# Kernel optimization log

Hardware: AMD Instinct MI355X
Metric: run time of the kernel (lower is better)

## Reference

```python
import jax, jax.numpy as jnp
import numpy as np

B, T, D, H = 4, 2048, 1024, 16
DK = D // H
LN_EPS = 1e-5


def setup_inputs() -> dict:
    key = jax.random.key(0)
    ks = jax.random.split(key, 12)
    s = 1.0 / np.sqrt(D)
    inp = {
        'x': jax.random.normal(ks[0], (B, T, D), jnp.float32),
        'Wq': jax.random.normal(ks[1], (D, D), jnp.float32) * s,
        'bq': jnp.zeros((D,), jnp.float32),
        'Wk': jax.random.normal(ks[2], (D, D), jnp.float32) * s,
        'bk': jnp.zeros((D,), jnp.float32),
        'Wv': jax.random.normal(ks[3], (D, D), jnp.float32) * s,
        'bv': jnp.zeros((D,), jnp.float32),
        'Wo': jax.random.normal(ks[4], (D, D), jnp.float32) * s,
        'bo': jnp.zeros((D,), jnp.float32),
        'ln_g': jnp.ones((D,), jnp.float32),
        'ln_b': jnp.zeros((D,), jnp.float32),
    }
    return inp


def reference(x, Wq, bq, Wk, bk, Wv, bv, Wo, bo, ln_g, ln_b):
    b, t, d = x.shape
    scale = jnp.sqrt(jnp.asarray(DK, x.dtype))
    # QKV projections -> [b, h, t, dk]
    q = (x @ Wq + bq).reshape(b, t, H, DK).transpose(0, 2, 1, 3)
    k = (x @ Wk + bk).reshape(b, t, H, DK).transpose(0, 2, 1, 3)
    v = (x @ Wv + bv).reshape(b, t, H, DK).transpose(0, 2, 1, 3)
    scores = jnp.einsum('bhqd,bhkd->bhqk', q, k) / scale  # [b,h,t,t]
    mask = jnp.tril(jnp.ones((t, t), x.dtype))[None, None]  # [1,1,t,t]
    neg = jnp.finfo(x.dtype).min
    scores = jnp.where(mask == 0, neg, scores)
    attn = jax.nn.softmax(scores, axis=-1)
    # mask-renormalize (as in the torch module)
    attn = attn * mask
    denom = attn.sum(-1, keepdims=True)
    attn = jnp.where(denom > 0, attn / denom, jnp.zeros_like(attn))
    ctx = jnp.einsum('bhqk,bhkd->bhqd', attn, v)  # [b,h,t,dk]
    ctx = ctx.transpose(0, 2, 1, 3).reshape(b, t, d)
    out = ctx @ Wo + bo
    y = out + x  # residual
    mu = y.mean(-1, keepdims=True)
    var = ((y - mu) ** 2).mean(-1, keepdims=True)
    return (y - mu) / jnp.sqrt(var + LN_EPS) * ln_g + ln_b
```

## Files before the change

### kernel.cpp

```cpp
#include <hip/hip_runtime.h>


using u16 = unsigned short;
using u32 = unsigned int;
typedef _Float16 f16x8 __attribute__((ext_vector_type(8)));
typedef __fp16 h16x2 __attribute__((ext_vector_type(2)));
typedef float f32x4 __attribute__((ext_vector_type(4)));
typedef unsigned short u16x8 __attribute__((ext_vector_type(8)));
typedef unsigned short u16x4 __attribute__((ext_vector_type(4)));
typedef unsigned int u32x4 __attribute__((ext_vector_type(4)));

template <bool B> struct BoolTag { static constexpr bool v = B; };

__device__ inline u16 f2h_bits(float f) {
    _Float16 h = (_Float16)f;
    return __builtin_bit_cast(u16, h);
}
__device__ inline float h2f(u16 u) {
    return (float)__builtin_bit_cast(_Float16, u);
}

__device__ __forceinline__ void gload16(const void* g, void* l) {
    __builtin_amdgcn_global_load_lds(
        (const __attribute__((address_space(1))) void*)g,
        (__attribute__((address_space(3))) void*)l, 16, 0, 0);
}

__global__ __launch_bounds__(256) void convert_kernel(
    const float* __restrict__ x, u16* __restrict__ xb,
    const float* __restrict__ W0, const float* __restrict__ W1,
    const float* __restrict__ W2, const float* __restrict__ W3,
    u16* __restrict__ Wt) {
    __shared__ float ts[64][68];
    const int bid = blockIdx.x, tid = threadIdx.x;
    if (bid < 4096) {
        size_t i = ((size_t)bid * 256 + tid) * 8;
        float4 a = *(const float4*)(x + i);
        float4 b = *(const float4*)(x + i + 4);
        u16x8 o;
        o[0] = f2h_bits(a.x); o[1] = f2h_bits(a.y); o[2] = f2h_bits(a.z); o[3] = f2h_bits(a.w);
        o[4] = f2h_bits(b.x); o[5] = f2h_bits(b.y); o[6] = f2h_bits(b.z); o[7] = f2h_bits(b.w);
        *(u16x8*)(xb + i) = o;
        return;
    }
    const int wb = bid - 4096;
    const int z = wb >> 8, rem = wb & 255;
    const float* W = z == 0 ? W0 : (z == 1 ? W1 : (z == 2 ? W2 : W3));
    u16* Wo = Wt + (size_t)z * 1048576;
    const int k0 = (rem >> 4) * 64, n0 = (rem & 15) * 64;
    const int rr = tid >> 3, c = tid & 7;
#pragma unroll
    for (int p = 0; p < 2; p++) {
        int k = p * 32 + rr;
        float4 u = *(const float4*)(W + (size_t)(k0 + k) * 1024 + n0 + c * 8);
        float4 w = *(const float4*)(W + (size_t)(k0 + k) * 1024 + n0 + c * 8 + 4);
        *(float4*)&ts[k][c * 8] = u;
        *(float4*)&ts[k][c * 8 + 4] = w;
    }
    __syncthreads();
#pragma unroll
    for (int p = 0; p < 2; p++) {
        int n = p * 32 + rr;
        u16 o[8];
#pragma unroll
        for (int j = 0; j < 8; j++) o[j] = f2h_bits(ts[c * 8 + j][n]);
        *(u16x8*)(Wo + (size_t)(n0 + n) * 1024 + k0 + c * 8) = *(u16x8*)o;
    }
}

template <int MODE>
__global__ __launch_bounds__(256) void gemm128_kernel(
    const u16* __restrict__ A, const u16* __restrict__ Wt,
    const float* __restrict__ b0, const float* __restrict__ b1,
    const float* __restrict__ b2, u16* __restrict__ qo, u16* __restrict__ ko,
    u16* __restrict__ vt) {
    constexpr int NBY = (MODE == 0) ? 24 : 8;
    __shared__ u16 SH[32768];

    const int bid = blockIdx.x;
    const int cpx = (MODE == 0) ? 192 : 64;
    const int swz = (bid & 7) * cpx + (bid >> 3);
    const int bx = swz / NBY, by = swz % NBY;
    const size_t row0 = (size_t)bx * 128;
    const size_t col0 = (size_t)by * 128;

    const int tid = threadIdx.x, lane = tid & 63;
    const int wid = tid >> 6, wm = wid >> 1, wn = wid & 1;
    const int l15 = lane & 15, lg = lane >> 4;
    const int rr = tid >> 3, c8 = tid & 7;
    const int scw = (c8 ^ (rr & 7)) * 8;

    f32x4 acc[4][4] = {};

    auto stage_tile = [&](int kt, int p) {
        const int k0 = kt * 64;
        u16* dA = SH + p * 8192;
        u16* dB = SH + 16384 + p * 8192;
#pragma unroll
        for (int g = 0; g < 4; g++) {
            gload16(A + (row0 + g * 32 + rr) * 1024 + k0 + scw,
                    dA + (g * 256 + tid) * 8);
            gload16(Wt + (col0 + g * 32 + rr) * 1024 + k0 + scw,
                    dB + (g * 256 + tid) * 8);
        }
    };

    auto ldops = [&](int p, int kcv, f16x8* Af, f16x8* Bf) {
        const u16* bA = SH + p * 8192;
        const u16* bB = SH + 16384 + p * 8192;
        const int swo = ((kcv * 4 + lg) ^ (l15 & 7)) * 8;
#pragma unroll
        for (int n = 0; n < 4; n++)
            Bf[n] = *(const f16x8*)(bB + (wn * 64 + n * 16 + l15) * 64 + swo);
#pragma unroll
        for (int m = 0; m < 4; m++)
            Af[m] = *(const f16x8*)(bA + (wm * 64 + m * 16 + l15) * 64 + swo);
    };

    auto domfma = [&](const f16x8* Af, const f16x8* Bf) {
        __builtin_amdgcn_s_setprio(1);
#pragma unroll
        for (int m = 0; m < 4; m++)
#pragma unroll
            for (int n = 0; n < 4; n++)
                acc[m][n] = __builtin_amdgcn_mfma_f32_16x16x32_f16(
                    Af[m], Bf[n], acc[m][n], 0, 0, 0);
        __builtin_amdgcn_s_setprio(0);
    };

    stage_tile(0, 0);
    asm volatile("s_waitcnt vmcnt(0)" ::: "memory");
    __builtin_amdgcn_sched_barrier(0);
    __builtin_amdgcn_s_barrier();

#pragma unroll 1
    for (int t = 0; t < 16; t++) {
        const int cp = t & 1, np = (t + 1) & 1;
        f16x8 af[4], bf[4];
        ldops(cp, 0, af, bf);
        if (t < 15) stage_tile(t + 1, np);
        __builtin_amdgcn_sched_barrier(0);
        __builtin_amdgcn_s_barrier();
        asm volatile("s_waitcnt lgkmcnt(0)" ::: "memory");
        __builtin_amdgcn_sched_barrier(0);
        domfma(af, bf);
        __builtin_amdgcn_sched_barrier(0);
        __builtin_amdgcn_s_barrier();
        ldops(cp, 1, af, bf);
        if (t < 15) asm volatile("s_waitcnt vmcnt(0)" ::: "memory");
        __builtin_amdgcn_sched_barrier(0);
        __builtin_amdgcn_s_barrier();
        asm volatile("s_waitcnt lgkmcnt(0)" ::: "memory");
        __builtin_amdgcn_sched_barrier(0);
        domfma(af, bf);
        __builtin_amdgcn_sched_barrier(0);
        if (t < 15) __builtin_amdgcn_s_barrier();
    }

    if (MODE == 0) {
        const int zsel = by >> 3;
        if (zsel < 2) {
            u16* ob = zsel == 0 ? qo : ko;
            const float* bias = zsel == 0 ? b0 : b1;
            const float qs = zsel == 0 ? 0.18033688f : 1.0f;
#pragma unroll
            for (int m = 0; m < 4; m++) {
#pragma unroll
                for (int n = 0; n < 4; n++) {
                    size_t col = col0 + wn * 64 + n * 16 + l15;
                    size_t colz = col & 1023;
                    float bb = bias[colz];
#pragma unroll
                    for (int r = 0; r < 4; r++) {
                        size_t row = row0 + wm * 64 + m * 16 + lg * 4 + r;
                        ob[row * 1024 + colz] = f2h_bits((acc[m][n][r] + bb) * qs);
                    }
                }
            }
        } else {
            u16* TL = SH;
            const int dz0 = (by - 16) * 128;
            __syncthreads();
#pragma unroll
            for (int m = 0; m < 4; m++) {
#pragma unroll
                for (int n = 0; n < 4; n++) {
                    int cl = wn * 64 + n * 16 + l15;
                    float bb = b2[dz0 + cl];
#pragma unroll
                    for (int r = 0; r < 4; r++) {
                        int rl = wm * 64 + m * 16 + lg * 4 + r;
                        TL[cl * 134 + rl] = f2h_bits(acc[m][n][r] + bb);
                    }
                }
            }
            __syncthreads();
            const int vcl = tid >> 1, th = tid & 1;
            const int b = (int)(row0 >> 11);
            const int tloc = (int)(row0 & 2047);
            size_t vrow = (size_t)b * 1024 + dz0 + vcl;
#pragma unroll
            for (int j = 0; j < 8; j++)
                *(u16x8*)(vt + vrow * 2048 + tloc + th * 64 + j * 8) =
                    *(const u16x8*)(TL + vcl * 134 + th * 64 + j * 8);
        }
    } else {
        u16* yo = qo;
        const u16* xres = ko;
#pragma unroll
        for (int m = 0; m < 4; m++) {
#pragma unroll
            for (int n = 0; n < 4; n++) {
                size_t col = col0 + wn * 64 + n * 16 + l15;
                float bb = b0[col];
#pragma unroll
                for (int r = 0; r < 4; r++) {
                    size_t row = row0 + wm * 64 + m * 16 + lg * 4 + r;
                    size_t idx = row * 1024 + col;
                    yo[idx] = f2h_bits(acc[m][n][r] + bb + h2f(xres[idx]));
                }
            }
        }
    }
}

__global__ __launch_bounds__(512) void attn_kernel(const u16* __restrict__ Q,
                                                   const u16* __restrict__ Kb,
                                                   const u16* __restrict__ Vt,
                                                   u16* __restrict__ ctx) {
    __shared__ u16 Ks[2][128 * 64];
    __shared__ u16 Vs[2][64 * 128];

    const int i = (int)blockIdx.x;
    const int bh = i & 63;
    const int sel = (i >> 6) & 3;
    const int qb = (i < 256) ? (7 - sel) : sel;
    const int b = bh >> 4, h = bh & 15;
    const int tid = threadIdx.x, lane = tid & 63, wid = tid >> 6;
    const int l15 = lane & 15, lg = lane >> 4;
    const int q0w = qb * 256 + wid * 32;
    const int send = qb * 256;

    const int rr = tid >> 3, c8 = tid & 7;
    const int scw = (c8 ^ (rr & 7)) * 8;
    const int vr = tid >> 4, vc = tid & 15;
    const int scv = (vc ^ (vr & 15)) * 8;
    const size_t kbase = ((size_t)b * 2048) * 1024 + h * 64 + scw;
    const size_t vbase0 = ((size_t)bh * 64 + vr) * 2048 + scv;
    const size_t vbase1 = ((size_t)bh * 64 + vr + 32) * 2048 + scv;

    f16x8 qv[2][2];
#pragma unroll
    for (int qf = 0; qf < 2; qf++) {
        size_t qoff = ((size_t)b * 2048 + q0w + qf * 16 + l15) * 1024 + h * 64 + lg * 8;
        qv[qf][0] = *(const f16x8*)(Q + qoff);
        qv[qf][1] = *(const f16x8*)(Q + qoff + 32);
    }

    const int swk0 = (lg ^ (l15 & 7)) * 8;
    const int swk1 = ((4 + lg) ^ (l15 & 7)) * 8;

    const h16x2 one2 = {(__fp16)1.0f, (__fp16)1.0f};

    f32x4 acc[2][4] = {};
    float psum[2] = {0.0f, 0.0f};

    auto stage = [&](int s, int bf) {
        gload16(Kb + kbase + (size_t)(s + rr) * 1024, Ks[bf] + tid * 8);
        gload16(Kb + kbase + (size_t)(s + rr + 64) * 1024, Ks[bf] + (512 + tid) * 8);
        gload16(Vt + vbase0 + s, Vs[bf] + tid * 8);
        gload16(Vt + vbase1 + s, Vs[bf] + (512 + tid) * 8);
    };

    auto body = [&](int s, int bf, auto maskc) {
        constexpr bool MASK = decltype(maskc)::v;
        u32 W[2][8][2];
#pragma unroll
        for (int c = 0; c < 8; c++) {
            const u16* kp = Ks[bf] + (c * 16 + l15) * 64;
            f16x8 kf0 = *(const f16x8*)(kp + swk0);
            f16x8 kf1 = *(const f16x8*)(kp + swk1);
#pragma unroll
            for (int qf = 0; qf < 2; qf++) {
                f32x4 z = {};
                z = __builtin_amdgcn_mfma_f32_16x16x32_f16(kf0, qv[qf][0], z, 0, 0, 0);
                z = __builtin_amdgcn_mfma_f32_16x16x32_f16(kf1, qv[qf][1], z, 0, 0, 0);
                float p0 = __builtin_amdgcn_exp2f(z[0]);
                float p1 = __builtin_amdgcn_exp2f(z[1]);
                float p2 = __builtin_amdgcn_exp2f(z[2]);
                float p3 = __builtin_amdgcn_exp2f(z[3]);
                if (MASK) {
                    int kk = s + c * 16 + lg * 4;
                    int qq = q0w + qf * 16 + l15;
                    p0 = (kk + 0 <= qq) ? p0 : 0.0f;
                    p1 = (kk + 1 <= qq) ? p1 : 0.0f;
                    p2 = (kk + 2 <= qq) ? p2 : 0.0f;
                    p3 = (kk + 3 <= qq) ? p3 : 0.0f;
                }
                h16x2 w0 = __builtin_amdgcn_cvt_pkrtz(p0, p1);
                h16x2 w1 = __builtin_amdgcn_cvt_pkrtz(p2, p3);
                psum[qf] = __builtin_amdgcn_fdot2(w0, one2, psum[qf], false);
                psum[qf] = __builtin_amdgcn_fdot2(w1, one2, psum[qf], false);
                W[qf][c][0] = __builtin_bit_cast(u32, w0);
                W[qf][c][1] = __builtin_bit_cast(u32, w1);
            }
        }
        f16x8 pa0[2][2], pa1[2][2];
#pragma unroll
        for (int qf = 0; qf < 2; qf++) {
#pragma unroll
            for (int hf = 0; hf < 2; hf++) {
                const int c0 = hf * 4;
                auto sA = __builtin_amdgcn_permlane32_swap(W[qf][c0][0], W[qf][c0 + 1][0], false, false);
                auto tA = __builtin_amdgcn_permlane16_swap(sA[0], sA[1], false, false);
                auto sB = __builtin_amdgcn_permlane32_swap(W[qf][c0][1], W[qf][c0 + 1][1], false, false);
                auto tB = __builtin_amdgcn_permlane16_swap(sB[0], sB[1], false, false);
                u32x4 v0 = {tA[0], tB[0], tA[1], tB[1]};
                pa0[qf][hf] = __builtin_bit_cast(f16x8, v0);
                auto sC = __builtin_amdgcn_permlane32_swap(W[qf][c0 + 2][0], W[qf][c0 + 3][0], false, false);
                auto tC = __builtin_amdgcn_permlane16_swap(sC[0], sC[1], false, false);
                auto sD = __builtin_amdgcn_permlane32_swap(W[qf][c0 + 2][1], W[qf][c0 + 3][1], false, false);
                auto tD = __builtin_amdgcn_permlane16_swap(sD[0], sD[1], false, false);
                u32x4 v1 = {tC[0], tD[0], tC[1], tD[1]};
                pa1[qf][hf] = __builtin_bit_cast(f16x8, v1);
            }
        }
        __builtin_amdgcn_s_setprio(1);
#pragma unroll
        for (int dt = 0; dt < 4; dt++) {
            const u16* vp = Vs[bf] + (dt * 16 + l15) * 128;
#pragma unroll
            for (int hf = 0; hf < 2; hf++) {
                f16x8 vf0 = *(const f16x8*)(vp + ((hf * 8 + lg) ^ l15) * 8);
                f16x8 vf1 = *(const f16x8*)(vp + ((hf * 8 + 4 + lg) ^ l15) * 8);
#pragma unroll
                for (int qf = 0; qf < 2; qf++) {
                    acc[qf][dt] = __builtin_amdgcn_mfma_f32_16x16x32_f16(
                        pa0[qf][hf], vf0, acc[qf][dt], 0, 0, 0);
                    acc[qf][dt] = __builtin_amdgcn_mfma_f32_16x16x32_f16(
                        pa1[qf][hf], vf1, acc[qf][dt], 0, 0, 0);
                }
            }
        }
        __builtin_amdgcn_s_setprio(0);
    };

    stage(0, 0);
    stage(128, 1);
    asm volatile("s_waitcnt vmcnt(4)" ::: "memory");
    __builtin_amdgcn_sched_barrier(0);
    __builtin_amdgcn_s_barrier();

    int cur = 0;
#pragma unroll 1
    for (int s = 0; s < send; s += 128) {
        body(s, cur, BoolTag<false>{});
        __builtin_amdgcn_sched_barrier(0);
        __builtin_amdgcn_s_barrier();
        stage(s + 256, cur);
        asm volatile("s_waitcnt vmcnt(4)" ::: "memory");
        __builtin_amdgcn_sched_barrier(0);
        __builtin_amdgcn_s_barrier();
        cur ^= 1;
    }
    body(send, cur, BoolTag<true>{});
    __builtin_amdgcn_sched_barrier(0);
    __builtin_amdgcn_s_barrier();
    asm volatile("s_waitcnt vmcnt(0)" ::: "memory");
    __builtin_amdgcn_sched_barrier(0);
    __builtin_amdgcn_s_barrier();
    if (wid >= 4) body(send + 128, cur ^ 1, BoolTag<true>{});

#pragma unroll
    for (int qf = 0; qf < 2; qf++) {
        psum[qf] += __shfl_xor(psum[qf], 16);
        psum[qf] += __shfl_xor(psum[qf], 32);
    }
#pragma unroll
    for (int qf = 0; qf < 2; qf++) {
        float inv = 1.0f / psum[qf];
#pragma unroll
        for (int r = 0; r < 4; r++) {
            float ir = __shfl(inv, lg * 4 + r);
            size_t row = (size_t)b * 2048 + q0w + qf * 16 + lg * 4 + r;
#pragma unroll
            for (int dt = 0; dt < 4; dt++)
                ctx[row * 1024 + h * 64 + dt * 16 + l15] = f2h_bits(acc[qf][dt][r] * ir);
        }
    }
}

__global__ __launch_bounds__(256) void ln_kernel(const u16* __restrict__ y,
                                                 const float* __restrict__ g,
                                                 const float* __restrict__ bb,
                                                 float* __restrict__ out) {
    const int r = blockIdx.x, tid = threadIdx.x;
    u16x4 v4 = *(const u16x4*)(y + (size_t)r * 1024 + tid * 4);
    float vx = h2f(v4[0]), vy = h2f(v4[1]), vz = h2f(v4[2]), vw = h2f(v4[3]);
    float s = vx + vy + vz + vw;
    float sq = vx * vx + vy * vy + vz * vz + vw * vw;
#pragma unroll
    for (int ofs = 1; ofs < 64; ofs <<= 1) {
        s += __shfl_xor(s, ofs);
        sq += __shfl_xor(sq, ofs);
    }
    __shared__ float as[4], aq[4];
    if ((tid & 63) == 0) { as[tid >> 6] = s; aq[tid >> 6] = sq; }
    __syncthreads();
    s = as[0] + as[1] + as[2] + as[3];
    sq = aq[0] + aq[1] + aq[2] + aq[3];
    float mu = s * (1.0f / 1024.0f);
    float var = sq * (1.0f / 1024.0f) - mu * mu;
    float rstd = rsqrtf(var + 1e-5f);
    float4 gv = *(const float4*)(g + tid * 4);
    float4 bv = *(const float4*)(bb + tid * 4);
    float4 o4;
    o4.x = (vx - mu) * rstd * gv.x + bv.x;
    o4.y = (vy - mu) * rstd * gv.y + bv.y;
    o4.z = (vz - mu) * rstd * gv.z + bv.z;
    o4.w = (vw - mu) * rstd * gv.w + bv.w;
    *(float4*)(out + (size_t)r * 1024 + tid * 4) = o4;
}

extern "C" void kernel_launch(void* const* d_in, const int* in_sizes, int n_in,
                              void* d_out, int out_size, void* d_ws, size_t ws_size,
                              hipStream_t stream) {
    const float* x  = (const float*)d_in[0];
    const float* Wq = (const float*)d_in[1];
    const float* bq = (const float*)d_in[2];
    const float* Wk = (const float*)d_in[3];
    const float* bk = (const float*)d_in[4];
    const float* Wv = (const float*)d_in[5];
    const float* bv = (const float*)d_in[6];
    const float* Wo = (const float*)d_in[7];
    const float* bo = (const float*)d_in[8];
    const float* lg = (const float*)d_in[9];
    const float* lb = (const float*)d_in[10];
    float* out = (float*)d_out;

    char* ws = (char*)d_ws;
    u16* xb = (u16*)(ws + 0);
    u16* wt = (u16*)(ws + 16777216);
    u16* q  = (u16*)(ws + 25165824);
    u16* k  = (u16*)(ws + 41943040);
    u16* vt = (u16*)(ws + 75497472);
    u16* cx = (u16*)(ws + 92274688);
    u16* y16 = (u16*)(ws + 109051904);

    convert_kernel<<<5120, 256, 0, stream>>>(x, xb, Wq, Wk, Wv, Wo, wt);

    gemm128_kernel<0><<<1536, 256, 0, stream>>>(xb, wt, bq, bk, bv, q, k, vt);
    attn_kernel<<<512, 512, 0, stream>>>(q, k, vt, cx);
    gemm128_kernel<1><<<512, 256, 0, stream>>>(cx, wt + 3145728, bo, nullptr,
                                               nullptr, y16, xb, nullptr);
    ln_kernel<<<8192, 256, 0, stream>>>(y16, lg, lb, out);
}
```

Before: 169.0 us.

## Give output-projection GEMM a dedicated 128x256 tile kernel with triple-buffered loads

Splits the templated GEMM into a QKV kernel and a new output-projection kernel. The new kernel uses 512 threads, 128x256 tiles (256 blocks) and a three-stage LDS ring that prefetches two k-tiles ahead in halves. The aim is more reuse of the A tile and deeper latency hiding for the Wo GEMM. In exchange it launches only 256 blocks, about one wave on the GPU, and uses much more LDS per block.

```diff
diff --git a/kernel.cpp b/kernel.cpp
--- a/kernel.cpp
+++ b/kernel.cpp
@@ -68,19 +68,16 @@
     }
 }
 
-template <int MODE>
-__global__ __launch_bounds__(256) void gemm128_kernel(
+__global__ __launch_bounds__(256) void gemm_qkv128_kernel(
     const u16* __restrict__ A, const u16* __restrict__ Wt,
     const float* __restrict__ b0, const float* __restrict__ b1,
     const float* __restrict__ b2, u16* __restrict__ qo, u16* __restrict__ ko,
     u16* __restrict__ vt) {
-    constexpr int NBY = (MODE == 0) ? 24 : 8;
     __shared__ u16 SH[32768];
 
     const int bid = blockIdx.x;
-    const int cpx = (MODE == 0) ? 192 : 64;
-    const int swz = (bid & 7) * cpx + (bid >> 3);
-    const int bx = swz / NBY, by = swz % NBY;
+    const int swz = (bid & 7) * 192 + (bid >> 3);
+    const int bx = swz / 24, by = swz % 24;
     const size_t row0 = (size_t)bx * 128;
     const size_t col0 = (size_t)by * 128;
 
@@ -157,68 +154,161 @@
         if (t < 15) __builtin_amdgcn_s_barrier();
     }
 
-    if (MODE == 0) {
-        const int zsel = by >> 3;
-        if (zsel < 2) {
-            u16* ob = zsel == 0 ? qo : ko;
-            const float* bias = zsel == 0 ? b0 : b1;
-            const float qs = zsel == 0 ? 0.18033688f : 1.0f;
-#pragma unroll
-            for (int m = 0; m < 4; m++) {
-#pragma unroll
-                for (int n = 0; n < 4; n++) {
-                    size_t col = col0 + wn * 64 + n * 16 + l15;
-                    size_t colz = col & 1023;
-                    float bb = bias[colz];
-#pragma unroll
-                    for (int r = 0; r < 4; r++) {
-                        size_t row = row0 + wm * 64 + m * 16 + lg * 4 + r;
-                        ob[row * 1024 + colz] = f2h_bits((acc[m][n][r] + bb) * qs);
-                    }
+    const int zsel = by >> 3;
+    if (zsel < 2) {
+        u16* ob = zsel == 0 ? qo : ko;
+        const float* bias = zsel == 0 ? b0 : b1;
+        const float qs = zsel == 0 ? 0.18033688f : 1.0f;
+#pragma unroll
+        for (int m = 0; m < 4; m++) {
+#pragma unroll
+            for (int n = 0; n < 4; n++) {
+                size_t col = col0 + wn * 64 + n * 16 + l15;
+                size_t colz = col & 1023;
+                float bb = bias[colz];
+#pragma unroll
+                for (int r = 0; r < 4; r++) {
+                    size_t row = row0 + wm * 64 + m * 16 + lg * 4 + r;
+                    ob[row * 1024 + colz] = f2h_bits((acc[m][n][r] + bb) * qs);
                 }
             }
-        } else {
-            u16* TL = SH;
-            const int dz0 = (by - 16) * 128;
-            __syncthreads();
-#pragma unroll
-            for (int m = 0; m < 4; m++) {
-#pragma unroll
-                for (int n = 0; n < 4; n++) {
-                    int cl = wn * 64 + n * 16 + l15;
-                    float bb = b2[dz0 + cl];
-#pragma unroll
-                    for (int r = 0; r < 4; r++) {
-                        int rl = wm * 64 + m * 16 + lg * 4 + r;
-                        TL[cl * 134 + rl] = f2h_bits(acc[m][n][r] + bb);
-                    }
+        }
+    } else {
+        u16* TL = SH;
+        const int dz0 = (by - 16) * 128;
+        __syncthreads();
+#pragma unroll
+        for (int m = 0; m < 4; m++) {
+#pragma unroll
+            for (int n = 0; n < 4; n++) {
+                int cl = wn * 64 + n * 16 + l15;
+                float bb = b2[dz0 + cl];
+#pragma unroll
+                for (int r = 0; r < 4; r++) {
+                    int rl = wm * 64 + m * 16 + lg * 4 + r;
+                    TL[cl * 134 + rl] = f2h_bits(acc[m][n][r] + bb);
                 }
             }
-            __syncthreads();
-            const int vcl = tid >> 1, th = tid & 1;
-            const int b = (int)(row0 >> 11);
-            const int tloc = (int)(row0 & 2047);
-            size_t vrow = (size_t)b * 1024 + dz0 + vcl;
-#pragma unroll
-            for (int j = 0; j < 8; j++)
-                *(u16x8*)(vt + vrow * 2048 + tloc + th * 64 + j * 8) =
-                    *(const u16x8*)(TL + vcl * 134 + th * 64 + j * 8);
-        }
-    } else {
-        u16* yo = qo;
-        const u16* xres = ko;
-#pragma unroll
-        for (int m = 0; m < 4; m++) {
-#pragma unroll
-            for (int n = 0; n < 4; n++) {
-                size_t col = col0 + wn * 64 + n * 16 + l15;
-                float bb = b0[col];
-#pragma unroll
-                for (int r = 0; r < 4; r++) {
-                    size_t row = row0 + wm * 64 + m * 16 + lg * 4 + r;
-                    size_t idx = row * 1024 + col;
-                    yo[idx] = f2h_bits(acc[m][n][r] + bb + h2f(xres[idx]));
-                }
+        }
+        __syncthreads();
+        const int vcl = tid >> 1, th = tid & 1;
+        const int b = (int)(row0 >> 11);
+        const int tloc = (int)(row0 & 2047);
+        size_t vrow = (size_t)b * 1024 + dz0 + vcl;
+#pragma unroll
+        for (int j = 0; j < 8; j++)
+            *(u16x8*)(vt + vrow * 2048 + tloc + th * 64 + j * 8) =
+                *(const u16x8*)(TL + vcl * 134 + th * 64 + j * 8);
+    }
+}
+
+__global__ __launch_bounds__(512) void gemm_wo_kernel(
+    const u16* __restrict__ A, const u16* __restrict__ Wt,
+    const float* __restrict__ b0, u16* __restrict__ yo,
+    const u16* __restrict__ xres) {
+    __shared__ u16 As[3][128 * 64];
+    __shared__ u16 Bs[3][256 * 64];
+
+    const int bid = blockIdx.x;
+    const int swz = (bid & 7) * 32 + (bid >> 3);
+    const int bx = swz / 4, by = swz % 4;
+    const size_t row0 = (size_t)bx * 128;
+    const size_t col0 = (size_t)by * 256;
+
+    const int tid = threadIdx.x, lane = tid & 63;
+    const int wid = tid >> 6, wm = wid >> 2, wn = wid & 3;
+    const int l15 = lane & 15, lg = lane >> 4;
+    const int rr = tid >> 3, c8 = tid & 7;
+    const int scw = (c8 ^ (rr & 7)) * 8;
+
+    f32x4 acc[4][4] = {};
+
+    auto stage_half = [&](int kt, u16* dA, u16* dB, int h) {
+        const int k0 = kt * 64;
+        if (h == 0) {
+            gload16(A + (row0 + rr) * 1024 + k0 + scw, dA + tid * 8);
+            gload16(Wt + (col0 + rr) * 1024 + k0 + scw, dB + tid * 8);
+            gload16(Wt + (col0 + 64 + rr) * 1024 + k0 + scw, dB + (512 + tid) * 8);
+        } else {
+            gload16(A + (row0 + 64 + rr) * 1024 + k0 + scw, dA + (512 + tid) * 8);
+            gload16(Wt + (col0 + 128 + rr) * 1024 + k0 + scw, dB + (1024 + tid) * 8);
+            gload16(Wt + (col0 + 192 + rr) * 1024 + k0 + scw, dB + (1536 + tid) * 8);
+        }
+    };
+
+    auto ldops = [&](const u16* bA, const u16* bB, int kcv, f16x8* Af, f16x8* Bf) {
+        const int swo = ((kcv * 4 + lg) ^ (l15 & 7)) * 8;
+#pragma unroll
+        for (int n = 0; n < 4; n++)
+            Bf[n] = *(const f16x8*)(bB + (wn * 64 + n * 16 + l15) * 64 + swo);
+#pragma unroll
+        for (int m = 0; m < 4; m++)
+            Af[m] = *(const f16x8*)(bA + (wm * 64 + m * 16 + l15) * 64 + swo);
+    };
+
+    auto domfma = [&](const f16x8* Af, const f16x8* Bf) {
+        __builtin_amdgcn_s_setprio(1);
+#pragma unroll
+        for (int m = 0; m < 4; m++)
+#pragma unroll
+            for (int n = 0; n < 4; n++)
+                acc[m][n] = __builtin_amdgcn_mfma_f32_16x16x32_f16(
+                    Af[m], Bf[n], acc[m][n], 0, 0, 0);
+        __builtin_amdgcn_s_setprio(0);
+    };
+
+    u16 *pA = &As[0][0], *pnA = &As[1][0], *ppA = &As[2][0];
+    u16 *pB = &Bs[0][0], *pnB = &Bs[1][0], *ppB = &Bs[2][0];
+
+    stage_half(0, pA, pB, 0);
+    stage_half(0, pA, pB, 1);
+    stage_half(1, pnA, pnB, 0);
+    stage_half(1, pnA, pnB, 1);
+    asm volatile("s_waitcnt vmcnt(6)" ::: "memory");
+    __builtin_amdgcn_sched_barrier(0);
+    __builtin_amdgcn_s_barrier();
+
+#pragma unroll 1
+    for (int t = 0; t < 16; t++) {
+        f16x8 af[4], bf[4];
+        ldops(pA, pB, 0, af, bf);
+        if (t < 14) stage_half(t + 2, ppA, ppB, 0);
+        __builtin_amdgcn_sched_barrier(0);
+        __builtin_amdgcn_s_barrier();
+        asm volatile("s_waitcnt lgkmcnt(0)" ::: "memory");
+        __builtin_amdgcn_sched_barrier(0);
+        domfma(af, bf);
+        __builtin_amdgcn_sched_barrier(0);
+        __builtin_amdgcn_s_barrier();
+        ldops(pA, pB, 1, af, bf);
+        if (t < 14) stage_half(t + 2, ppA, ppB, 1);
+        if (t < 14)       asm volatile("s_waitcnt vmcnt(6)" ::: "memory");
+        else if (t == 14) asm volatile("s_waitcnt vmcnt(0)" ::: "memory");
+        __builtin_amdgcn_sched_barrier(0);
+        __builtin_amdgcn_s_barrier();
+        asm volatile("s_waitcnt lgkmcnt(0)" ::: "memory");
+        __builtin_amdgcn_sched_barrier(0);
+        domfma(af, bf);
+        __builtin_amdgcn_sched_barrier(0);
+        if (t < 15) {
+            __builtin_amdgcn_s_barrier();
+            u16* tp;
+            tp = pA; pA = pnA; pnA = ppA; ppA = tp;
+            tp = pB; pB = pnB; pnB = ppB; ppB = tp;
+        }
+    }
+
+#pragma unroll
+    for (int m = 0; m < 4; m++) {
+#pragma unroll
+        for (int n = 0; n < 4; n++) {
+            size_t col = col0 + wn * 64 + n * 16 + l15;
+            float bb = b0[col];
+#pragma unroll
+            for (int r = 0; r < 4; r++) {
+                size_t row = row0 + wm * 64 + m * 16 + lg * 4 + r;
+                size_t idx = row * 1024 + col;
+                yo[idx] = f2h_bits(acc[m][n][r] + bb + h2f(xres[idx]));
             }
         }
     }
@@ -449,9 +539,8 @@
 
     convert_kernel<<<5120, 256, 0, stream>>>(x, xb, Wq, Wk, Wv, Wo, wt);
 
-    gemm128_kernel<0><<<1536, 256, 0, stream>>>(xb, wt, bq, bk, bv, q, k, vt);
+    gemm_qkv128_kernel<<<1536, 256, 0, stream>>>(xb, wt, bq, bk, bv, q, k, vt);
     attn_kernel<<<512, 512, 0, stream>>>(q, k, vt, cx);
-    gemm128_kernel<1><<<512, 256, 0, stream>>>(cx, wt + 3145728, bo, nullptr,
-                                               nullptr, y16, xb, nullptr);
+    gemm_wo_kernel<<<256, 512, 0, stream>>>(cx, wt + 3145728, bo, y16, xb);
     ln_kernel<<<8192, 256, 0, stream>>>(y16, lg, lb, out);
 }
```

Result: no change. 169.7 us (+0.4%).
